# Performance work log

Measured on AMD Instinct MI355X. Metric: run time of the kernel, lower is better.

The kernel has to match this reference:

```python
import jax, jax.numpy as jnp
import numpy as np

B, S, H = 2, 2048, 2048
NUM_HEADS, HEAD_DIM = 16, 128
SOFTMAX_SHIFT = 12


def _int_project(x, w_i8, b_i32, out_shift):
    # x: [..., in] int32, w_i8: [in, out] int8, b_i32: [out] int32
    y = jnp.matmul(x.astype(jnp.int32), w_i8.astype(jnp.int32))
    y = y + b_i32
    return jnp.right_shift(y, out_shift)  # arithmetic shift on signed int32


def setup_inputs() -> dict:
    key = jax.random.key(0)
    ks = jax.random.split(key, 9)
    x_i32 = jax.random.randint(ks[0], (B, S, H), 0, 256, dtype=jnp.int32)
    def w(k):
        return jax.random.randint(k, (H, H), -127, 128, dtype=jnp.int32).astype(jnp.int8)
    def b(k):
        return jax.random.randint(k, (H,), -64, 64, dtype=jnp.int32)
    return {
        "x_i32": x_i32,
        "wq": w(ks[1]), "bq": b(ks[2]),
        "wk": w(ks[3]), "bk": b(ks[4]),
        "wv": w(ks[5]), "bv": b(ks[6]),
        "wo": w(ks[7]), "bo": b(ks[8]),
    }


def reference(x_i32, wq, bq, wk, bk, wv, bv, wo, bo):
    bsz, seq, hidden = x_i32.shape

    def heads(t):  # [b, s, h] -> [b, nh, s, hd]
        return t.reshape(bsz, seq, NUM_HEADS, HEAD_DIM).transpose(0, 2, 1, 3)

    q = heads(_int_project(x_i32, wq, bq, 6))
    k = heads(_int_project(x_i32, wk, bk, 6))
    v = heads(_int_project(x_i32, wv, bv, 6))

    # int32 scores [b, nh, s, s], halved by arithmetic right shift
    scores = jnp.right_shift(jnp.einsum("bhqd,bhkd->bhqk", q, k), 1)

    idx = jnp.arange(seq)
    causal = idx[:, None] >= idx[None, :]  # [s, s]
    neg = jnp.int32(-(1 << 20))
    masked = jnp.where(causal[None, None], scores, neg)

    # clamp-softmax surrogate: subtract row max, clamp(x + 256, 0, 2^12 - 1)
    shifted = masked - jnp.max(masked, axis=-1, keepdims=True)
    attn = jnp.clip(shifted + 256, 0, (1 << SOFTMAX_SHIFT) - 1)

    context = jnp.right_shift(jnp.einsum("bhqk,bhkd->bhqd", attn, v), SOFTMAX_SHIFT)
    context = context.transpose(0, 2, 1, 3).reshape(bsz, seq, hidden)
    return _int_project(context, wo, bo, 7)
```

## Files before the change

kernel.cpp:

```cpp
#include <hip/hip_runtime.h>
#include <stdint.h>


#define SEQ   2048
#define HID   2048
#define NHEAD 16
#define HDIM  128
#define NB    2
#define NEGV  (-(1 << 20))
#define PLANE 8388608
#define WSZ   4194304
#define BHSTR 262144

#define AS1 __attribute__((address_space(1)))
#define AS3 __attribute__((address_space(3)))

typedef int v4i __attribute__((ext_vector_type(4)));

__device__ __forceinline__ v4i mfma_i8(v4i a, v4i b, v4i c) {
  return __builtin_amdgcn_mfma_i32_16x16x64_i8(a, b, c, 0, 0, 0);
}

__device__ __forceinline__ void gl16(const char* g, char* l) {
  __builtin_amdgcn_global_load_lds((const AS1 uint32_t*)g, (AS3 uint32_t*)l, 16, 0, 0);
}

__device__ __forceinline__ void limb3(int v, int& l0, int& l1, int& l2) {
  l0 = (v << 24) >> 24;
  int t = (v - l0) >> 8;
  l1 = (t << 24) >> 24;
  l2 = (t - l1) >> 8;
}

__device__ __forceinline__ int sext4(int x) {
  return ((x << 24) >> 24) + ((x << 16) >> 24) + ((x << 8) >> 24) + (x >> 24);
}

__global__ __launch_bounds__(256) void xpack(const int* __restrict__ X, char* __restrict__ Xs8)
{
  const int i = blockIdx.x * 256 + threadIdx.x;
  int4 v = ((const int4*)X)[i];
  uint32_t b = (uint32_t)((v.x - 128) & 255)
             | ((uint32_t)((v.y - 128) & 255) << 8)
             | ((uint32_t)((v.z - 128) & 255) << 16)
             | ((uint32_t)((v.w - 128) & 255) << 24);
  ((uint32_t*)Xs8)[i] = b;
}

__global__ __launch_bounds__(256) void wpack(const int* __restrict__ Wq, const int* __restrict__ Wk,
                                             const int* __restrict__ Wv, const int* __restrict__ Wo,
                                             char* __restrict__ WtQKV, char* __restrict__ WtO)
{
  __shared__ char Ws[128 * 144];
  const int z = blockIdx.z;
  const int* W = (z == 0) ? Wq : (z == 1) ? Wk : (z == 2) ? Wv : Wo;
  char* Wt = (z < 3) ? (WtQKV + (size_t)z * WSZ) : WtO;
  const int k0 = blockIdx.x * 128, n0 = blockIdx.y * 128;
  const int t = threadIdx.x;
  const int lr = t >> 1, lc = (t & 1) * 64;
  const int* wp = W + (size_t)(k0 + lr) * HID + n0 + lc;
#pragma unroll
  for (int i = 0; i < 16; i++) {
    int4 v = *(const int4*)(wp + 4 * i);
    uint32_t pb = (uint32_t)(v.x & 255) | ((uint32_t)(v.y & 255) << 8)
                | ((uint32_t)(v.z & 255) << 16) | ((uint32_t)(v.w & 255) << 24);
    *(uint32_t*)&Ws[lr * 144 + lc + 4 * i] = pb;
  }
  __syncthreads();
  const int nl = t >> 1, kh = (t & 1) * 64;
  char* op = Wt + (size_t)(n0 + nl) * HID + k0 + kh;
#pragma unroll
  for (int w = 0; w < 16; w++) {
    uint32_t u = 0;
#pragma unroll
    for (int j = 0; j < 4; j++)
      u |= ((uint32_t)(unsigned char)Ws[(kh + w * 4 + j) * 144 + nl]) << (8 * j);
    *(uint32_t*)(op + 4 * w) = u;
  }
}

__global__ __launch_bounds__(256) void csum(const char* __restrict__ WtQKV,
                                            const int* __restrict__ Bq, const int* __restrict__ Bk,
                                            const int* __restrict__ Bv, int* __restrict__ bias2)
{
  const int id = blockIdx.x;
  const int z = id >> 9;
  const int n = ((id & 511) << 2) + (threadIdx.x >> 6);
  const int lane = threadIdx.x & 63;
  const int4* p = (const int4*)(WtQKV + (size_t)z * WSZ + (size_t)n * HID + lane * 32);
  int4 a = p[0], b4 = p[1];
  int vals[8] = {a.x, a.y, a.z, a.w, b4.x, b4.y, b4.z, b4.w};
  int s = 0;
#pragma unroll
  for (int i = 0; i < 8; i++) s += sext4(vals[i]);
#pragma unroll
  for (int m = 1; m < 64; m <<= 1) s += __shfl_xor(s, m);
  if (lane == 0) {
    const int* B = (z == 0) ? Bq : (z == 1) ? Bk : Bv;
    bias2[z * HID + n] = (int)((uint32_t)B[n] + ((uint32_t)s << 7));
  }
}

__global__ __launch_bounds__(256, 3) void qkv_mfma(const char* __restrict__ Xs8,
                                                   const char* __restrict__ WtQKV,
                                                   const int* __restrict__ bias2,
                                                   char* __restrict__ QL, char* __restrict__ KL,
                                                   int* __restrict__ VR, int* __restrict__ PS)
{
  __shared__ __align__(16) char smem[33792];
  const int id = blockIdx.x;
  const int n0 = (id & 15) * 128;
  const int zm = id >> 4;
  const int z  = zm >> 5;
  const int m0 = (zm & 31) * 128;
  const char* Wt = WtQKV + (size_t)z * WSZ;
  const int* b2 = bias2 + z * HID;

  const int t = threadIdx.x, wave = t >> 6, lane = t & 63;
  const int r16 = lane & 15, quad = lane >> 4;
  const int wm = (wave >> 1) * 64, wn = (wave & 1) * 64;

  const char* AgJ[4]; const char* BgJ[4];
  char* AlJ[4]; char* BlJ[4];
#pragma unroll
  for (int j = 0; j < 4; j++) {
    const int s = j * 256 + t;
    const int row = s >> 3;
    const int cg = (s & 7) ^ (row & 7);
    AgJ[j] = Xs8 + (size_t)(m0 + row) * HID + cg * 16;
    BgJ[j] = Wt  + (size_t)(n0 + row) * HID + cg * 16;
    AlJ[j] = smem + j * 4096 + wave * 1024;
    BlJ[j] = smem + 16384 + j * 4096 + wave * 1024;
  }

  v4i acc[4][4];
#pragma unroll
  for (int i = 0; i < 4; i++)
#pragma unroll
    for (int j = 0; j < 4; j++) acc[i][j] = (v4i){0, 0, 0, 0};

  for (int k0 = 0; k0 < HID; k0 += 128) {
#pragma unroll
    for (int j = 0; j < 4; j++) gl16(AgJ[j] + k0, AlJ[j]);
#pragma unroll
    for (int j = 0; j < 4; j++) gl16(BgJ[j] + k0, BlJ[j]);
    __syncthreads();
#pragma unroll
    for (int kk = 0; kk < 2; kk++) {
      const int xo = ((kk * 4 + quad) ^ (r16 & 7)) * 16;
      v4i Af[4], Bf[4];
#pragma unroll
      for (int mt = 0; mt < 4; mt++)
        Af[mt] = *(const v4i*)(smem + (wm + mt * 16 + r16) * 128 + xo);
#pragma unroll
      for (int nt = 0; nt < 4; nt++)
        Bf[nt] = *(const v4i*)(smem + 16384 + (wn + nt * 16 + r16) * 128 + xo);
#pragma unroll
      for (int mt = 0; mt < 4; mt++)
#pragma unroll
        for (int nt = 0; nt < 4; nt++)
          acc[mt][nt] = mfma_i8(Af[mt], Bf[nt], acc[mt][nt]);
    }
    __syncthreads();
  }

  int bvv[4];
#pragma unroll
  for (int nt = 0; nt < 4; nt++) bvv[nt] = b2[n0 + wn + nt * 16 + r16];

  const int h  = id & 15;
  const int b  = m0 >> 11;
  const int s0 = m0 & 2047;
  const int bh = b * 16 + h;
  const int myhalf = wave >> 1;

  if (z <= 1) {
    char* dplane = (z == 0) ? QL : KL;
#pragma unroll
    for (int half = 0; half < 2; half++) {
      __syncthreads();
      if (myhalf == half) {
#pragma unroll
        for (int mt = 0; mt < 4; mt++)
#pragma unroll
          for (int nt = 0; nt < 4; nt++) {
            const int col = wn + nt * 16 + r16;
#pragma unroll
            for (int r = 0; r < 4; r++) {
              const int y = ((int)((uint32_t)acc[mt][nt][r] + (uint32_t)bvv[nt])) >> 6;
              int l0, l1, l2; limb3(y, l0, l1, l2);
              const int off = (mt * 16 + quad * 4 + r) * 144 + col;
              smem[off]         = (char)l0;
              smem[9216 + off]  = (char)l1;
              smem[18432 + off] = (char)l2;
            }
          }
      }
      __syncthreads();
      if (t < 192) {
        const int l = t >> 6, rc = t & 63;
        const char* src = &smem[l * 9216 + rc * 144];
        char* dp = dplane + (size_t)l * PLANE + (size_t)bh * BHSTR
                 + (size_t)(s0 + half * 64 + rc) * 128;
#pragma unroll
        for (int j = 0; j < 8; j++)
          *(int4*)(dp + j * 16) = *(const int4*)(src + j * 16);
      }
    }
  } else {
    int* s32 = (int*)smem;
#pragma unroll
    for (int half = 0; half < 2; half++) {
      __syncthreads();
      if (myhalf == half) {
#pragma unroll
        for (int mt = 0; mt < 4; mt++)
#pragma unroll
          for (int nt = 0; nt < 4; nt++) {
            const int col = wn + nt * 16 + r16;
#pragma unroll
            for (int r = 0; r < 4; r++) {
              const int y = ((int)((uint32_t)acc[mt][nt][r] + (uint32_t)bvv[nt])) >> 6;
              s32[(mt * 16 + quad * 4 + r) * 132 + col] = y;
            }
          }
      }
      __syncthreads();
      {
        const int rr = t >> 2, cs = (t & 3) * 32;
        int* vp = VR + (size_t)bh * (SEQ * HDIM) + (size_t)(s0 + half * 64 + rr) * HDIM + cs;
        const int* sp = s32 + rr * 132 + cs;
#pragma unroll
        for (int j = 0; j < 8; j++)
          *(int4*)(vp + 4 * j) = *(const int4*)(sp + 4 * j);
      }
      if (t < 128) {
        uint32_t a = 0;
        for (int j = 0; j < 64; j++) a += (uint32_t)s32[j * 132 + t];
        PS[((size_t)bh * 32 + (s0 >> 6) + half) * 128 + t] = (int)a;
      }
    }
  }
}

__global__ __launch_bounds__(128) void suf(const int* __restrict__ PS, int* __restrict__ SUF)
{
  const int bh = blockIdx.x, d = threadIdx.x;
  SUF[((size_t)bh * 33 + 32) * 128 + d] = 0;
  uint32_t acc = 0;
  for (int tt = 31; tt >= 0; tt--) {
    acc += (uint32_t)PS[((size_t)bh * 32 + tt) * 128 + d];
    SUF[((size_t)bh * 33 + tt) * 128 + d] = (int)acc;
  }
}

__global__ __launch_bounds__(512, 4) void attn_mfma(const char* __restrict__ QL,
    const char* __restrict__ KL, const int* __restrict__ VR,
    const int* __restrict__ SUF, char* __restrict__ CL)
{
  __shared__ __align__(16) char smK[24576];
  __shared__ int   candS[64 * 32];
  __shared__ unsigned short candK[64 * 32];
  __shared__ int   mrow[64];
  __shared__ int   cnt[64];

  const int t = threadIdx.x, w = t >> 6, lane = t & 63;
  const int r16 = lane & 15, quad = lane >> 4;
  const int bid = blockIdx.x;
  const int bh = bid & 31;
  const int tile = 31 - (bid >> 5);
  const int q0 = tile * 64;
  const int b = bh >> 4, h = bh & 15;
  const char* QLb = QL + (size_t)bh * BHSTR;
  const char* KLb = KL + (size_t)bh * BHSTR;
  const int g = w >> 1, p = w & 1;
  const int wq = q0 + g * 16;
  const int ktlast = q0 >> 6;

  if (t < 64) { mrow[t] = (int)0x80000000; cnt[t] = 0; }

  const int srow = w * 8 + (lane >> 3);
  const int schunk = (lane & 7) ^ (lane >> 3);
  const char* kg = KLb + (size_t)srow * 128 + schunk * 16;

  v4i Aq[3][2];
  {
    const char* qb = QLb + (size_t)(wq + r16) * 128 + quad * 16;
#pragma unroll
    for (int l = 0; l < 3; l++)
#pragma unroll
      for (int c = 0; c < 2; c++)
        Aq[l][c] = *(const v4i*)(qb + (size_t)l * PLANE + c * 64);
  }

  int qrow[4], mr[4];
#pragma unroll
  for (int r = 0; r < 4; r++) {
    qrow[r] = wq + quad * 4 + r;
    mr[r] = (qrow[r] == SEQ - 1) ? (int)0x80000000 : NEGV;
  }

  const v4i vzero = (v4i){0, 0, 0, 0};
  const int sw0 = ((0 * 4 + quad) ^ (r16 & 7)) * 16;
  const int sw1 = ((1 * 4 + quad) ^ (r16 & 7)) * 16;

  for (int kt = 0; kt <= ktlast; kt++) {
    const size_t kb = (size_t)kt * 8192;
#pragma unroll
    for (int l = 0; l < 3; l++)
      gl16(kg + (size_t)l * PLANE + kb, smK + l * 8192 + w * 1024);
    __syncthreads();

    const bool last = (kt == ktlast);
    int sc[2][4];
#pragma unroll
    for (int nt2 = 0; nt2 < 2; nt2++) {
      const int nt = 2 * p + nt2;
      const char* kbase = smK + (nt * 16 + r16) * 128;
      v4i B[3][2];
#pragma unroll
      for (int l = 0; l < 3; l++) {
        B[l][0] = *(const v4i*)(kbase + l * 8192 + sw0);
        B[l][1] = *(const v4i*)(kbase + l * 8192 + sw1);
      }
      v4i c0, c1, c2, c3;
      c0 = mfma_i8(Aq[0][0], B[0][0], vzero);
      c0 = mfma_i8(Aq[0][1], B[0][1], c0);
      c1 = mfma_i8(Aq[0][0], B[1][0], vzero);
      c1 = mfma_i8(Aq[0][1], B[1][1], c1);
      c1 = mfma_i8(Aq[1][0], B[0][0], c1);
      c1 = mfma_i8(Aq[1][1], B[0][1], c1);
      c2 = mfma_i8(Aq[0][0], B[2][0], vzero);
      c2 = mfma_i8(Aq[0][1], B[2][1], c2);
      c2 = mfma_i8(Aq[1][0], B[1][0], c2);
      c2 = mfma_i8(Aq[1][1], B[1][1], c2);
      c2 = mfma_i8(Aq[2][0], B[0][0], c2);
      c2 = mfma_i8(Aq[2][1], B[0][1], c2);
      c3 = mfma_i8(Aq[1][0], B[2][0], vzero);
      c3 = mfma_i8(Aq[1][1], B[2][1], c3);
      c3 = mfma_i8(Aq[2][0], B[1][0], c3);
      c3 = mfma_i8(Aq[2][1], B[1][1], c3);
#pragma unroll
      for (int r = 0; r < 4; r++) {
        const uint32_t u = (uint32_t)c0[r] + ((uint32_t)c1[r] << 8)
                         + ((uint32_t)c2[r] << 16) + ((uint32_t)c3[r] << 24);
        sc[nt2][r] = ((int)u) >> 1;
      }
    }
    __syncthreads();

#pragma unroll
    for (int r = 0; r < 4; r++) {
      int mv = (int)0x80000000;
#pragma unroll
      for (int nt2 = 0; nt2 < 2; nt2++) {
        const int gj = kt * 64 + (2 * p + nt2) * 16 + r16;
        const bool valid = !last || (gj <= qrow[r]);
        const int s = valid ? sc[nt2][r] : (int)0x80000000;
        mv = s > mv ? s : mv;
      }
#pragma unroll
      for (int msk = 1; msk < 16; msk <<= 1) {
        const int o = __shfl_xor(mv, msk);
        mv = o > mv ? o : mv;
      }
      mr[r] = mv > mr[r] ? mv : mr[r];
    }
#pragma unroll
    for (int nt2 = 0; nt2 < 2; nt2++) {
      const int gj = kt * 64 + (2 * p + nt2) * 16 + r16;
#pragma unroll
      for (int r = 0; r < 4; r++) {
        const bool valid = !last || (gj <= qrow[r]);
        if (valid && sc[nt2][r] >= mr[r] - 255) {
          const int lrow = g * 16 + quad * 4 + r;
          const int slot = atomicAdd(&cnt[lrow], 1);
          if (slot < 32) {
            candS[lrow * 32 + slot] = sc[nt2][r];
            candK[lrow * 32 + slot] = (unsigned short)gj;
          }
        }
      }
    }
  }
  if (r16 == 0) {
#pragma unroll
    for (int r = 0; r < 4; r++)
      atomicMax(&mrow[g * 16 + quad * 4 + r], mr[r]);
  }
  __syncthreads();

  const int* VRb = VR + (size_t)bh * (SEQ * HDIM);
  const int t64 = q0 >> 6;
  const uint32_t* sufp = (const uint32_t*)(SUF + ((size_t)bh * 33 + t64 + 1) * 128);
  const int d0 = lane * 2;
  const uint32_t ts0 = sufp[d0], ts1 = sufp[d0 + 1];
  const int blkend = (t64 + 1) * 64;

#pragma unroll 1
  for (int i = 0; i < 8; i++) {
    const int lrow = w * 8 + i;
    const int qr = q0 + lrow;
    const int m = mrow[lrow];
    int c = cnt[lrow]; c = c > 32 ? 32 : c;
    uint32_t O0 = 0, O1 = 0;
    for (int idx = 0; idx < c; idx++) {
      const int s = candS[lrow * 32 + idx];
      const int a = s - m + 256;
      if (a > 0) {
        const int key = candK[lrow * 32 + idx];
        const int2 v = *(const int2*)(VRb + (size_t)key * HDIM + d0);
        O0 += (uint32_t)a * (uint32_t)v.x;
        O1 += (uint32_t)a * (uint32_t)v.y;
      }
    }
    int wmv = 0;
    if (m <= NEGV + 255) wmv = NEGV - m + 256;
    if (wmv > 0) {
      uint32_t T0 = ts0, T1 = ts1;
      for (int j = qr + 1; j < blkend; j++) {
        const int2 v = *(const int2*)(VRb + (size_t)j * HDIM + d0);
        T0 += (uint32_t)v.x; T1 += (uint32_t)v.y;
      }
      O0 += (uint32_t)wmv * T0;
      O1 += (uint32_t)wmv * T1;
    }
    const int ctx0 = ((int)O0) >> 12;
    const int ctx1 = ((int)O1) >> 12;
    int a0, a1, a2, e0, e1, e2;
    limb3(ctx0, a0, a1, a2);
    limb3(ctx1, e0, e1, e2);
    const size_t rowb = (size_t)(b * SEQ + qr) * 2048 + (size_t)h * 128 + d0;
    *(unsigned short*)(CL + rowb)             = (unsigned short)((a0 & 255) | ((e0 & 255) << 8));
    *(unsigned short*)(CL + PLANE + rowb)     = (unsigned short)((a1 & 255) | ((e1 & 255) << 8));
    *(unsigned short*)(CL + 2 * (size_t)PLANE + rowb)
                                              = (unsigned short)((a2 & 255) | ((e2 & 255) << 8));
  }
}

__global__ __launch_bounds__(256, 3) void out_mfma(const char* __restrict__ CL,
                                                   const char* __restrict__ WtO,
                                                   const int* __restrict__ Bo,
                                                   int* __restrict__ Out)
{
  __shared__ __align__(16) char smem[40960];
  const int id = blockIdx.x;
  const int n0 = (id & 15) * 128;
  const int m0 = (id >> 4) * 64;

  const int t = threadIdx.x, wave = t >> 6, lane = t & 63;
  const int wm = (wave >> 1) * 32, wn = (wave & 1) * 64;
  const int r16 = lane & 15, quad = lane >> 4;

  const char* AgJ[3][2]; char* AlJ[3][2];
  const char* BgJ[4];   char* BlJ[4];
#pragma unroll
  for (int j = 0; j < 2; j++) {
    const int s = j * 256 + t;
    const int row = s >> 3;
    const int cg = (s & 7) ^ (row & 7);
#pragma unroll
    for (int l = 0; l < 3; l++) {
      AgJ[l][j] = CL + (size_t)l * PLANE + (size_t)(m0 + row) * HID + cg * 16;
      AlJ[l][j] = smem + l * 8192 + j * 4096 + wave * 1024;
    }
  }
#pragma unroll
  for (int j = 0; j < 4; j++) {
    const int s = j * 256 + t;
    const int row = s >> 3;
    const int cg = (s & 7) ^ (row & 7);
    BgJ[j] = WtO + (size_t)(n0 + row) * HID + cg * 16;
    BlJ[j] = smem + 24576 + j * 4096 + wave * 1024;
  }

  v4i acc[3][2][4];
#pragma unroll
  for (int l = 0; l < 3; l++)
#pragma unroll
    for (int i = 0; i < 2; i++)
#pragma unroll
      for (int j = 0; j < 4; j++) acc[l][i][j] = (v4i){0, 0, 0, 0};

  for (int k0 = 0; k0 < HID; k0 += 128) {
#pragma unroll
    for (int l = 0; l < 3; l++)
#pragma unroll
      for (int j = 0; j < 2; j++) gl16(AgJ[l][j] + k0, AlJ[l][j]);
#pragma unroll
    for (int j = 0; j < 4; j++) gl16(BgJ[j] + k0, BlJ[j]);
    __syncthreads();
#pragma unroll
    for (int kk = 0; kk < 2; kk++) {
      const int xo = ((kk * 4 + quad) ^ (r16 & 7)) * 16;
      v4i Af[3][2], Bf[4];
#pragma unroll
      for (int l = 0; l < 3; l++)
#pragma unroll
        for (int mt = 0; mt < 2; mt++)
          Af[l][mt] = *(const v4i*)(smem + l * 8192 + (wm + mt * 16 + r16) * 128 + xo);
#pragma unroll
      for (int nt = 0; nt < 4; nt++)
        Bf[nt] = *(const v4i*)(smem + 24576 + (wn + nt * 16 + r16) * 128 + xo);
#pragma unroll
      for (int l = 0; l < 3; l++)
#pragma unroll
        for (int mt = 0; mt < 2; mt++)
#pragma unroll
          for (int nt = 0; nt < 4; nt++)
            acc[l][mt][nt] = mfma_i8(Af[l][mt], Bf[nt], acc[l][mt][nt]);
    }
    __syncthreads();
  }

  int bov[4];
#pragma unroll
  for (int nt = 0; nt < 4; nt++) bov[nt] = Bo[n0 + wn + nt * 16 + r16];
#pragma unroll
  for (int mt = 0; mt < 2; mt++)
#pragma unroll
    for (int nt = 0; nt < 4; nt++)
#pragma unroll
      for (int r = 0; r < 4; r++) {
        uint32_t g = (uint32_t)acc[0][mt][nt][r]
                   + ((uint32_t)acc[1][mt][nt][r] << 8)
                   + ((uint32_t)acc[2][mt][nt][r] << 16)
                   + (uint32_t)bov[nt];
        Out[(size_t)(m0 + wm + mt * 16 + quad * 4 + r) * HID + n0 + wn + nt * 16 + r16] = ((int)g) >> 7;
      }
}

extern "C" void kernel_launch(void* const* d_in, const int* in_sizes, int n_in,
                              void* d_out, int out_size, void* d_ws, size_t ws_size,
                              hipStream_t stream)
{
  (void)in_sizes; (void)n_in; (void)out_size; (void)ws_size;

  const int* x  = (const int*)d_in[0];
  const int* wq = (const int*)d_in[1];
  const int* bq = (const int*)d_in[2];
  const int* wk = (const int*)d_in[3];
  const int* bk = (const int*)d_in[4];
  const int* wv = (const int*)d_in[5];
  const int* bv = (const int*)d_in[6];
  const int* wo = (const int*)d_in[7];
  const int* bo = (const int*)d_in[8];
  int* out = (int*)d_out;
  char* WS = (char*)d_ws;

  char* QLp   = WS + 0;
  char* KLp   = WS + 25165824;
  int*  VRp   = (int*)(WS + 50331648);
  int*  Sb    = (int*)(WS + 83886080);
  int*  PSb   = (int*)(WS + 84426752);
  int*  B2    = (int*)(WS + 84951040);
  char* WtO   = WS + 84975616;
  char* P     = WS + 89169920;
  char* WtQKV = P;
  char* Xs8   = P + 3 * (size_t)WSZ;
  char* CLp   = P;

  xpack<<<dim3(8192), dim3(256), 0, stream>>>(x, Xs8);
  wpack<<<dim3(16, 16, 4), dim3(256), 0, stream>>>(wq, wk, wv, wo, WtQKV, WtO);
  csum<<<dim3(1536), dim3(256), 0, stream>>>(WtQKV, bq, bk, bv, B2);
  qkv_mfma<<<dim3(1536), dim3(256), 0, stream>>>(Xs8, WtQKV, B2, QLp, KLp, VRp, PSb);
  suf<<<dim3(32), dim3(128), 0, stream>>>(PSb, Sb);
  attn_mfma<<<dim3(1024), dim3(512), 0, stream>>>(QLp, KLp, VRp, Sb, CLp);
  out_mfma<<<dim3(1024), dim3(256), 0, stream>>>(CLp, WtO, bo, out);
}
```

Measured before the change: 411.4 us.

## Fuse weight column-sum into wpack and process two key tiles per sync

Drops the separate csum kernel. Each wpack block now sums its transposed weight tile from shared memory and atomically adds the result (plus the bias once) into bias2, which a memset zeroes first. In attn_mfma the K-tile loop now loads two 64-key tiles into doubled shared memory per iteration, halving the number of barriers and load rounds. The cost is 48KB of K staging per block, which may lower occupancy below the launch bound of 4 blocks, plus global atomics on the bias.

```diff
diff --git a/kernel.cpp b/kernel.cpp
--- a/kernel.cpp
+++ b/kernel.cpp
@@ -49,7 +49,10 @@
 
 __global__ __launch_bounds__(256) void wpack(const int* __restrict__ Wq, const int* __restrict__ Wk,
                                              const int* __restrict__ Wv, const int* __restrict__ Wo,
-                                             char* __restrict__ WtQKV, char* __restrict__ WtO)
+                                             const int* __restrict__ Bq, const int* __restrict__ Bk,
+                                             const int* __restrict__ Bv,
+                                             char* __restrict__ WtQKV, char* __restrict__ WtO,
+                                             int* __restrict__ bias2)
 {
   __shared__ char Ws[128 * 144];
   const int z = blockIdx.z;
@@ -77,27 +80,17 @@
       u |= ((uint32_t)(unsigned char)Ws[(kh + w * 4 + j) * 144 + nl]) << (8 * j);
     *(uint32_t*)(op + 4 * w) = u;
   }
-}
-
-__global__ __launch_bounds__(256) void csum(const char* __restrict__ WtQKV,
-                                            const int* __restrict__ Bq, const int* __restrict__ Bk,
-                                            const int* __restrict__ Bv, int* __restrict__ bias2)
-{
-  const int id = blockIdx.x;
-  const int z = id >> 9;
-  const int n = ((id & 511) << 2) + (threadIdx.x >> 6);
-  const int lane = threadIdx.x & 63;
-  const int4* p = (const int4*)(WtQKV + (size_t)z * WSZ + (size_t)n * HID + lane * 32);
-  int4 a = p[0], b4 = p[1];
-  int vals[8] = {a.x, a.y, a.z, a.w, b4.x, b4.y, b4.z, b4.w};
-  int s = 0;
-#pragma unroll
-  for (int i = 0; i < 8; i++) s += sext4(vals[i]);
-#pragma unroll
-  for (int m = 1; m < 64; m <<= 1) s += __shfl_xor(s, m);
-  if (lane == 0) {
-    const int* B = (z == 0) ? Bq : (z == 1) ? Bk : Bv;
-    bias2[z * HID + n] = (int)((uint32_t)B[n] + ((uint32_t)s << 7));
+  if (z < 3) {
+    const int col = t >> 1, half = t & 1;
+    int s = 0;
+#pragma unroll 8
+    for (int j = 0; j < 64; j++)
+      s += (int)(signed char)Ws[(half * 64 + j) * 144 + col];
+    atomicAdd(&bias2[z * HID + n0 + col], (int)((uint32_t)s << 7));
+    if (k0 == 0 && half == 0) {
+      const int* B = (z == 0) ? Bq : (z == 1) ? Bk : Bv;
+      atomicAdd(&bias2[z * HID + n0 + col], B[n0 + col]);
+    }
   }
 }
 
@@ -258,7 +251,7 @@
     const char* __restrict__ KL, const int* __restrict__ VR,
     const int* __restrict__ SUF, char* __restrict__ CL)
 {
-  __shared__ __align__(16) char smK[24576];
+  __shared__ __align__(16) char smK[49152];
   __shared__ int   candS[64 * 32];
   __shared__ unsigned short candK[64 * 32];
   __shared__ int   mrow[64];
@@ -304,84 +297,96 @@
   const int sw0 = ((0 * 4 + quad) ^ (r16 & 7)) * 16;
   const int sw1 = ((1 * 4 + quad) ^ (r16 & 7)) * 16;
 
-  for (int kt = 0; kt <= ktlast; kt++) {
-    const size_t kb = (size_t)kt * 8192;
-#pragma unroll
-    for (int l = 0; l < 3; l++)
-      gl16(kg + (size_t)l * PLANE + kb, smK + l * 8192 + w * 1024);
+  for (int kt0 = 0; kt0 <= ktlast; kt0 += 2) {
+    const int jend = (kt0 + 1 <= ktlast) ? 2 : 1;
+    {
+      const size_t kb0 = (size_t)kt0 * 8192;
+#pragma unroll
+      for (int l = 0; l < 3; l++)
+        gl16(kg + (size_t)l * PLANE + kb0, smK + l * 8192 + w * 1024);
+      if (jend == 2) {
+#pragma unroll
+        for (int l = 0; l < 3; l++)
+          gl16(kg + (size_t)l * PLANE + kb0 + 8192, smK + 24576 + l * 8192 + w * 1024);
+      }
+    }
     __syncthreads();
 
-    const bool last = (kt == ktlast);
-    int sc[2][4];
-#pragma unroll
-    for (int nt2 = 0; nt2 < 2; nt2++) {
-      const int nt = 2 * p + nt2;
-      const char* kbase = smK + (nt * 16 + r16) * 128;
-      v4i B[3][2];
-#pragma unroll
-      for (int l = 0; l < 3; l++) {
-        B[l][0] = *(const v4i*)(kbase + l * 8192 + sw0);
-        B[l][1] = *(const v4i*)(kbase + l * 8192 + sw1);
-      }
-      v4i c0, c1, c2, c3;
-      c0 = mfma_i8(Aq[0][0], B[0][0], vzero);
-      c0 = mfma_i8(Aq[0][1], B[0][1], c0);
-      c1 = mfma_i8(Aq[0][0], B[1][0], vzero);
-      c1 = mfma_i8(Aq[0][1], B[1][1], c1);
-      c1 = mfma_i8(Aq[1][0], B[0][0], c1);
-      c1 = mfma_i8(Aq[1][1], B[0][1], c1);
-      c2 = mfma_i8(Aq[0][0], B[2][0], vzero);
-      c2 = mfma_i8(Aq[0][1], B[2][1], c2);
-      c2 = mfma_i8(Aq[1][0], B[1][0], c2);
-      c2 = mfma_i8(Aq[1][1], B[1][1], c2);
-      c2 = mfma_i8(Aq[2][0], B[0][0], c2);
-      c2 = mfma_i8(Aq[2][1], B[0][1], c2);
-      c3 = mfma_i8(Aq[1][0], B[2][0], vzero);
-      c3 = mfma_i8(Aq[1][1], B[2][1], c3);
-      c3 = mfma_i8(Aq[2][0], B[1][0], c3);
-      c3 = mfma_i8(Aq[2][1], B[1][1], c3);
+    for (int j = 0; j < jend; j++) {
+      const int kt = kt0 + j;
+      const char* smKj = smK + j * 24576;
+      const bool last = (kt == ktlast);
+      int sc[2][4];
+#pragma unroll
+      for (int nt2 = 0; nt2 < 2; nt2++) {
+        const int nt = 2 * p + nt2;
+        const char* kbase = smKj + (nt * 16 + r16) * 128;
+        v4i B[3][2];
+#pragma unroll
+        for (int l = 0; l < 3; l++) {
+          B[l][0] = *(const v4i*)(kbase + l * 8192 + sw0);
+          B[l][1] = *(const v4i*)(kbase + l * 8192 + sw1);
+        }
+        v4i c0, c1, c2, c3;
+        c0 = mfma_i8(Aq[0][0], B[0][0], vzero);
+        c0 = mfma_i8(Aq[0][1], B[0][1], c0);
+        c1 = mfma_i8(Aq[0][0], B[1][0], vzero);
+        c1 = mfma_i8(Aq[0][1], B[1][1], c1);
+        c1 = mfma_i8(Aq[1][0], B[0][0], c1);
+        c1 = mfma_i8(Aq[1][1], B[0][1], c1);
+        c2 = mfma_i8(Aq[0][0], B[2][0], vzero);
+        c2 = mfma_i8(Aq[0][1], B[2][1], c2);
+        c2 = mfma_i8(Aq[1][0], B[1][0], c2);
+        c2 = mfma_i8(Aq[1][1], B[1][1], c2);
+        c2 = mfma_i8(Aq[2][0], B[0][0], c2);
+        c2 = mfma_i8(Aq[2][1], B[0][1], c2);
+        c3 = mfma_i8(Aq[1][0], B[2][0], vzero);
+        c3 = mfma_i8(Aq[1][1], B[2][1], c3);
+        c3 = mfma_i8(Aq[2][0], B[1][0], c3);
+        c3 = mfma_i8(Aq[2][1], B[1][1], c3);
+#pragma unroll
+        for (int r = 0; r < 4; r++) {
+          const uint32_t u = (uint32_t)c0[r] + ((uint32_t)c1[r] << 8)
+                           + ((uint32_t)c2[r] << 16) + ((uint32_t)c3[r] << 24);
+          sc[nt2][r] = ((int)u) >> 1;
+        }
+      }
+
 #pragma unroll
       for (int r = 0; r < 4; r++) {
-        const uint32_t u = (uint32_t)c0[r] + ((uint32_t)c1[r] << 8)
-                         + ((uint32_t)c2[r] << 16) + ((uint32_t)c3[r] << 24);
-        sc[nt2][r] = ((int)u) >> 1;
-      }
-    }
-    __syncthreads();
-
-#pragma unroll
-    for (int r = 0; r < 4; r++) {
-      int mv = (int)0x80000000;
+        int mv = (int)0x80000000;
+#pragma unroll
+        for (int nt2 = 0; nt2 < 2; nt2++) {
+          const int gj = kt * 64 + (2 * p + nt2) * 16 + r16;
+          const bool valid = !last || (gj <= qrow[r]);
+          const int s = valid ? sc[nt2][r] : (int)0x80000000;
+          mv = s > mv ? s : mv;
+        }
+#pragma unroll
+        for (int msk = 1; msk < 16; msk <<= 1) {
+          const int o = __shfl_xor(mv, msk);
+          mv = o > mv ? o : mv;
+        }
+        mr[r] = mv > mr[r] ? mv : mr[r];
+      }
 #pragma unroll
       for (int nt2 = 0; nt2 < 2; nt2++) {
         const int gj = kt * 64 + (2 * p + nt2) * 16 + r16;
-        const bool valid = !last || (gj <= qrow[r]);
-        const int s = valid ? sc[nt2][r] : (int)0x80000000;
-        mv = s > mv ? s : mv;
-      }
-#pragma unroll
-      for (int msk = 1; msk < 16; msk <<= 1) {
-        const int o = __shfl_xor(mv, msk);
-        mv = o > mv ? o : mv;
-      }
-      mr[r] = mv > mr[r] ? mv : mr[r];
-    }
-#pragma unroll
-    for (int nt2 = 0; nt2 < 2; nt2++) {
-      const int gj = kt * 64 + (2 * p + nt2) * 16 + r16;
-#pragma unroll
-      for (int r = 0; r < 4; r++) {
-        const bool valid = !last || (gj <= qrow[r]);
-        if (valid && sc[nt2][r] >= mr[r] - 255) {
-          const int lrow = g * 16 + quad * 4 + r;
-          const int slot = atomicAdd(&cnt[lrow], 1);
-          if (slot < 32) {
-            candS[lrow * 32 + slot] = sc[nt2][r];
-            candK[lrow * 32 + slot] = (unsigned short)gj;
+#pragma unroll
+        for (int r = 0; r < 4; r++) {
+          const bool valid = !last || (gj <= qrow[r]);
+          if (valid && sc[nt2][r] >= mr[r] - 255) {
+            const int lrow = g * 16 + quad * 4 + r;
+            const int slot = atomicAdd(&cnt[lrow], 1);
+            if (slot < 32) {
+              candS[lrow * 32 + slot] = sc[nt2][r];
+              candK[lrow * 32 + slot] = (unsigned short)gj;
+            }
           }
         }
       }
     }
+    __syncthreads();
   }
   if (r16 == 0) {
 #pragma unroll
@@ -560,9 +565,10 @@
   char* Xs8   = P + 3 * (size_t)WSZ;
   char* CLp   = P;
 
+  hipMemsetAsync(B2, 0, 3 * HID * sizeof(int), stream);
   xpack<<<dim3(8192), dim3(256), 0, stream>>>(x, Xs8);
-  wpack<<<dim3(16, 16, 4), dim3(256), 0, stream>>>(wq, wk, wv, wo, WtQKV, WtO);
-  csum<<<dim3(1536), dim3(256), 0, stream>>>(WtQKV, bq, bk, bv, B2);
+  wpack<<<dim3(16, 16, 4), dim3(256), 0, stream>>>(wq, wk, wv, wo, bq, bk, bv,
+                                                   WtQKV, WtO, B2);
   qkv_mfma<<<dim3(1536), dim3(256), 0, stream>>>(Xs8, WtQKV, B2, QLp, KLp, VRp, PSb);
   suf<<<dim3(32), dim3(128), 0, stream>>>(PSb, Sb);
   attn_mfma<<<dim3(1024), dim3(512), 0, stream>>>(QLp, KLp, VRp, Sb, CLp);
```

Result: slower. 420.8 us (+2.3%).
